# Kernel tuning notes

Measured on AMD Instinct MI355X. Metric: run time of the kernel, lower is better.

## Reference

```python
import jax, jax.numpy as jnp
import numpy as np

IN_FEATURES = 1024
OUT_FEATURES = 1024
BATCH = 32
SEQ = 1024
EPS = 1e-8


def setup_inputs() -> dict:
    key = jax.random.key(0)
    k1, k2, k3 = jax.random.split(key, 3)
    Efou = jax.random.normal(k1, (BATCH, SEQ, IN_FEATURES), dtype=jnp.float32)
    y = jax.random.normal(k2, (BATCH, IN_FEATURES), dtype=jnp.float32)
    weight = jax.random.normal(k3, (IN_FEATURES, OUT_FEATURES), dtype=jnp.float32)
    return {"Efou": Efou, "y": y, "weight": weight}


def reference(Efou, y, weight):
    # scale = 1/sqrt(in_features)
    scale = 1.0 / np.sqrt(np.float32(weight.shape[0]))
    ys = y * scale  # (b, i) == per-sample column scaling of weight
    # Demodulation norm: sum_i (scale*W[i,o]*y[b,i])^2 = (ys^2) @ (W^2)
    d = jax.lax.rsqrt(jnp.einsum('bi,io->bo', ys * ys, weight * weight) + EPS)  # (b, o)
    # Efou @ (scale*W*y*d) == ((Efou*ys) @ W) * d  -- same math, avoids (b,i,o) weight
    out = jnp.einsum('bsi,io->bso', Efou * ys[:, None, :], weight) * d[:, None, :]
    return out
```

## Files before the change

### kernel.cpp

```cpp
#include <hip/hip_runtime.h>

#define AS1 __attribute__((address_space(1)))
#define AS3 __attribute__((address_space(3)))

typedef __bf16 bf16x8 __attribute__((ext_vector_type(8)));
typedef float f32x4 __attribute__((ext_vector_type(4)));
typedef unsigned short ushort8 __attribute__((ext_vector_type(8)));

__device__ __forceinline__ unsigned short f2bf(float f) {
  union { float f; unsigned u; } v; v.f = f;
  unsigned u = v.u;
  unsigned r = (u + 0x7fffu + ((u >> 16) & 1u)) >> 16;
  return (unsigned short)r;
}

__global__ __launch_bounds__(256) void prep_kernel(const float* __restrict__ y,
                                                   const float* __restrict__ W,
                                                   float* __restrict__ partial,
                                                   unsigned short* __restrict__ WT) {
  __shared__ float ysq[32][32];
  const int o = blockIdx.x * 256 + threadIdx.x;
  const int i0 = blockIdx.y * 32;
  for (int e = threadIdx.x; e < 1024; e += 256) {
    int il = e >> 5, b = e & 31;
    float t = y[b * 1024 + i0 + il] * 0.03125f;
    ysq[il][b] = t * t;
  }
  __syncthreads();

  f32x4 acc[8] = {};
  ushort8 wb[4];
#pragma unroll
  for (int il = 0; il < 32; ++il) {
    float w = W[(size_t)(i0 + il) * 1024 + o];
    wb[il >> 3][il & 7] = f2bf(w);
    float w2 = w * w;
#pragma unroll
    for (int b4 = 0; b4 < 8; ++b4) {
      f32x4 q = *(const f32x4*)&ysq[il][b4 * 4];
#pragma unroll
      for (int k = 0; k < 4; ++k) acc[b4][k] = fmaf(q[k], w2, acc[b4][k]);
    }
  }
  unsigned short* wt = WT + (size_t)o * 1024 + i0;
#pragma unroll
  for (int q = 0; q < 4; ++q) *(ushort8*)(wt + q * 8) = wb[q];
  float* p = partial + (size_t)blockIdx.y * 32768 + o;
#pragma unroll
  for (int b4 = 0; b4 < 8; ++b4)
#pragma unroll
    for (int k = 0; k < 4; ++k) p[(b4 * 4 + k) * 1024] = acc[b4][k];
}

__global__ __launch_bounds__(256) void dcalc_b_kernel(const float* __restrict__ partial,
                                                      float* __restrict__ dmod) {
  const int bo = blockIdx.x * 256 + threadIdx.x;
  float acc = 0.f;
#pragma unroll 8
  for (int is = 0; is < 32; ++is) acc += partial[(size_t)is * 32768 + bo];
  dmod[bo] = rsqrtf(acc + 1e-8f);
}

#define NT 16
#define LDS_TILE 65536

#define BAR __builtin_amdgcn_s_barrier()
#define LGKM0 asm volatile("s_waitcnt lgkmcnt(0)" ::: "memory")
#define VM(n) asm volatile("s_waitcnt vmcnt(" #n ")" ::: "memory")
#define SCHB __builtin_amdgcn_sched_barrier(0)
#define PRIO(x) __builtin_amdgcn_s_setprio(x)

#define STG_B(r, t, dst)                                                     \
  __builtin_amdgcn_global_load_lds(                                          \
      (const AS1 void*)(Ws + (size_t)(r) * 64 * 2048 + (t) * 128),           \
      (AS3 void*)((dst) + 32768 + (r) * 8192 + sldso), 16, 0, 0)

#define A_ISSUE(t)                                                           \
  {                                                                          \
    const float* asrc = Efou + (size_t)(m0 + argp * 4) * 1024 + (t) * 64 + k8; \
    _Pragma("unroll") for (int rr = 0; rr < 4; ++rr) {                       \
      pa[rr][0] = *(const f32x4*)(asrc + rr * 1024);                         \
      pa[rr][1] = *(const f32x4*)(asrc + rr * 1024 + 4);                     \
    }                                                                        \
    yv[0] = *(const f32x4*)(ysS + (t) * 64 + k8);                            \
    yv[1] = *(const f32x4*)(ysS + (t) * 64 + k8 + 4);                        \
  }

#define ACVT_ROW(dst, rr)                                                    \
  {                                                                          \
    const int row = argp * 4 + (rr);                                         \
    bf16x8 ov;                                                               \
    _Pragma("unroll") for (int q = 0; q < 4; ++q) {                          \
      ov[q] = (__bf16)(pa[rr][0][q] * yv[0][q]);                             \
      ov[q + 4] = (__bf16)(pa[rr][1][q] * yv[1][q]);                         \
    }                                                                        \
    *(bf16x8*)((dst) + row * 128 + ((kslot * 16) ^ ((row & 7) << 4))) = ov;  \
  }

#define RD_A(mh, mi, kk)                                                     \
  (*(const bf16x8*)(Ab + (wr * 128 + ((mh) * 4 + (mi)) * 16 + l15) * 128 +   \
                    ((((kk) * 64 + lhi * 16)) ^ swz_rd)))
#define RD_B(nh, ni, kk)                                                     \
  (*(const bf16x8*)(Bb + (wc * 64 + ((nh) * 2 + (ni)) * 16 + l15) * 128 +    \
                    ((((kk) * 64 + lhi * 16)) ^ swz_rd)))

#define LD_A(mh)                                                             \
  { _Pragma("unroll") for (int mi = 0; mi < 4; ++mi)                         \
      _Pragma("unroll") for (int kk = 0; kk < 2; ++kk)                       \
        a[mi][kk] = RD_A(mh, mi, kk); }
#define LD_B(nh)                                                             \
  { _Pragma("unroll") for (int ni = 0; ni < 2; ++ni)                         \
      _Pragma("unroll") for (int kk = 0; kk < 2; ++kk)                       \
        bfr[ni][kk] = RD_B(nh, ni, kk); }

#define MM(mh, nh)                                                           \
  do {                                                                       \
    _Pragma("unroll") for (int mi = 0; mi < 4; ++mi)                         \
      _Pragma("unroll") for (int ni = 0; ni < 2; ++ni)                       \
        _Pragma("unroll") for (int kk = 0; kk < 2; ++kk)                     \
          acc[(mh) * 4 + mi][(nh) * 2 + ni] =                                \
              __builtin_amdgcn_mfma_f32_16x16x32_bf16(                       \
                  a[mi][kk], bfr[ni][kk], acc[(mh) * 4 + mi][(nh) * 2 + ni], \
                  0, 0, 0);                                                  \
  } while (0)

__global__ __launch_bounds__(512, 2) void gemmf5_kernel(
    const float* __restrict__ Efou, const float* __restrict__ y,
    const unsigned short* __restrict__ WT, const float* __restrict__ dmod,
    float* __restrict__ out) {
  extern __shared__ char lds[];
  float* ysS = (float*)(lds + 2 * LDS_TILE);

  const int tid = threadIdx.x;
  const int bid = blockIdx.x;
  const int wg = (bid & 7) * 64 + (bid >> 3);
  const int bm = wg >> 2, bn = wg & 3;
  const int m0 = bm * 256, n0 = bn * 256;
  const int b = m0 >> 10;

  const int w = tid >> 6, l = tid & 63;
  const int wr = w >> 2, wc = w & 3;
  const int l15 = l & 15, lhi = l >> 4;
  const int swz_rd = (l15 & 7) << 4;

  const int kslot = tid & 7;
  const int k8 = kslot * 8;
  const int argp = tid >> 3;

  const int srow = tid >> 3;
  const int scb = ((tid & 7) << 4) ^ ((srow & 7) << 4);
  const char* Ws = (const char*)WT + (size_t)(n0 + srow) * 2048 + scb;
  const int sldso = tid * 16;

  f32x4 acc[8][4] = {};
  bf16x8 a[4][2], bfr[2][2];
  f32x4 pa[4][2], yv[2];

  {
    float2 yy = *(const float2*)(y + b * 1024 + tid * 2);
    ysS[2 * tid] = yy.x * 0.03125f;
    ysS[2 * tid + 1] = yy.y * 0.03125f;
  }
  __syncthreads();
  {
    char* d0 = lds;
    STG_B(0, 0, d0); STG_B(1, 0, d0); STG_B(2, 0, d0); STG_B(3, 0, d0);
    A_ISSUE(0);
    ACVT_ROW(d0, 0); ACVT_ROW(d0, 1); ACVT_ROW(d0, 2); ACVT_ROW(d0, 3);
  }
  VM(0); LGKM0; BAR;

  for (int t = 0; t < NT - 1; ++t) {
    const char* Ab = lds + (t & 1) * LDS_TILE;
    const char* Bb = Ab + 32768;
    char* dN = lds + ((t & 1) ^ 1) * LDS_TILE;
    const int t1 = t + 1;
    LD_A(0); LD_B(0);
    A_ISSUE(t1);
    STG_B(0, t1, dN); STG_B(1, t1, dN);
    BAR; LGKM0; SCHB; PRIO(1); MM(0, 0); PRIO(0); SCHB; BAR;
    LD_B(1);
    STG_B(2, t1, dN); STG_B(3, t1, dN);
    BAR; LGKM0; SCHB; PRIO(1); MM(0, 1); PRIO(0); SCHB; BAR;
    LD_A(1); LD_B(0);
    BAR; LGKM0; SCHB; PRIO(1);
    ACVT_ROW(dN, 0); ACVT_ROW(dN, 1);
    MM(1, 0);
    PRIO(0); SCHB; BAR;
    LD_B(1);
    BAR; LGKM0; SCHB; PRIO(1);
    ACVT_ROW(dN, 2); ACVT_ROW(dN, 3);
    MM(1, 1);
    PRIO(0); SCHB;
    VM(0);
    LGKM0;
    BAR;
  }

  {
    const char* Ab = lds + ((NT - 1) & 1) * LDS_TILE;
    const char* Bb = Ab + 32768;
    LD_A(0); LD_B(0);
    BAR; LGKM0; SCHB; PRIO(1); MM(0, 0); PRIO(0); SCHB; BAR;
    LD_B(1);
    BAR; LGKM0; SCHB; PRIO(1); MM(0, 1); PRIO(0); SCHB; BAR;
    LD_A(1); LD_B(0);
    BAR; LGKM0; SCHB; PRIO(1); MM(1, 0); PRIO(0); SCHB; BAR;
    LD_B(1);
    BAR; LGKM0; SCHB; PRIO(1); MM(1, 1); PRIO(0); SCHB;
  }

  const int col0 = n0 + wc * 64 + l15;
  float dv[4];
#pragma unroll
  for (int nf = 0; nf < 4; ++nf) dv[nf] = dmod[b * 1024 + col0 + nf * 16];
#pragma unroll
  for (int mf = 0; mf < 8; ++mf) {
#pragma unroll
    for (int j = 0; j < 4; ++j) {
      const int row = m0 + wr * 128 + mf * 16 + lhi * 4 + j;
      float* orow = out + (size_t)row * 1024 + col0;
#pragma unroll
      for (int nf = 0; nf < 4; ++nf) orow[nf * 16] = acc[mf][nf][j] * dv[nf];
    }
  }
}

extern "C" void kernel_launch(void* const* d_in, const int* in_sizes, int n_in,
                              void* d_out, int out_size, void* d_ws, size_t ws_size,
                              hipStream_t stream) {
  const float* Efou = (const float*)d_in[0];
  const float* y    = (const float*)d_in[1];
  const float* W    = (const float*)d_in[2];
  float* out = (float*)d_out;

  unsigned short* WT = (unsigned short*)d_ws;
  float* dpart       = (float*)(WT + (size_t)1024 * 1024);
  float* dmod        = dpart + (size_t)32 * 32768;

  hipFuncSetAttribute((const void*)gemmf5_kernel,
                      hipFuncAttributeMaxDynamicSharedMemorySize, 135168);

  prep_kernel<<<dim3(4, 32), 256, 0, stream>>>(y, W, dpart, WT);
  dcalc_b_kernel<<<128, 256, 0, stream>>>(dpart, dmod);
  gemmf5_kernel<<<512, 512, 135168, stream>>>(Efou, y, WT, dmod, out);
}
```

Measured before the change: 127.9 us.

## Load all B fragments once per tile and remove intermediate barriers

Loads both halves of the B fragments into registers at the start of each K-tile instead of reloading them for each A half. This halves the B LDS reads, and most intermediate barriers and waits in the main loop are removed, so MFMA phases run back-to-back. The cost is more vector registers held live, which could cause spills under the 2-blocks-per-CU launch bound, and less fine-grained interleaving of global staging with compute.

```diff
diff --git a/kernel.cpp b/kernel.cpp
--- a/kernel.cpp
+++ b/kernel.cpp
@@ -108,10 +108,11 @@
   { _Pragma("unroll") for (int mi = 0; mi < 4; ++mi)                         \
       _Pragma("unroll") for (int kk = 0; kk < 2; ++kk)                       \
         a[mi][kk] = RD_A(mh, mi, kk); }
-#define LD_B(nh)                                                             \
-  { _Pragma("unroll") for (int ni = 0; ni < 2; ++ni)                         \
-      _Pragma("unroll") for (int kk = 0; kk < 2; ++kk)                       \
-        bfr[ni][kk] = RD_B(nh, ni, kk); }
+#define LD_B_ALL                                                             \
+  { _Pragma("unroll") for (int nh = 0; nh < 2; ++nh)                         \
+      _Pragma("unroll") for (int ni = 0; ni < 2; ++ni)                       \
+        _Pragma("unroll") for (int kk = 0; kk < 2; ++kk)                     \
+          bfr[nh][ni][kk] = RD_B(nh, ni, kk); }
 
 #define MM(mh, nh)                                                           \
   do {                                                                       \
@@ -120,11 +121,11 @@
         _Pragma("unroll") for (int kk = 0; kk < 2; ++kk)                     \
           acc[(mh) * 4 + mi][(nh) * 2 + ni] =                                \
               __builtin_amdgcn_mfma_f32_16x16x32_bf16(                       \
-                  a[mi][kk], bfr[ni][kk], acc[(mh) * 4 + mi][(nh) * 2 + ni], \
-                  0, 0, 0);                                                  \
+                  a[mi][kk], bfr[nh][ni][kk],                                \
+                  acc[(mh) * 4 + mi][(nh) * 2 + ni], 0, 0, 0);               \
   } while (0)
 
-__global__ __launch_bounds__(512, 2) void gemmf5_kernel(
+__global__ __launch_bounds__(512, 2) void gemmf6_kernel(
     const float* __restrict__ Efou, const float* __restrict__ y,
     const unsigned short* __restrict__ WT, const float* __restrict__ dmod,
     float* __restrict__ out) {
@@ -153,7 +154,7 @@
   const int sldso = tid * 16;
 
   f32x4 acc[8][4] = {};
-  bf16x8 a[4][2], bfr[2][2];
+  bf16x8 a[4][2], bfr[2][2][2];
   f32x4 pa[4][2], yv[2];
 
   {
@@ -175,20 +176,14 @@
     const char* Bb = Ab + 32768;
     char* dN = lds + ((t & 1) ^ 1) * LDS_TILE;
     const int t1 = t + 1;
-    LD_A(0); LD_B(0);
+    LD_A(0); LD_B_ALL;
     A_ISSUE(t1);
-    STG_B(0, t1, dN); STG_B(1, t1, dN);
-    BAR; LGKM0; SCHB; PRIO(1); MM(0, 0); PRIO(0); SCHB; BAR;
-    LD_B(1);
-    STG_B(2, t1, dN); STG_B(3, t1, dN);
-    BAR; LGKM0; SCHB; PRIO(1); MM(0, 1); PRIO(0); SCHB; BAR;
-    LD_A(1); LD_B(0);
-    BAR; LGKM0; SCHB; PRIO(1);
+    STG_B(0, t1, dN); STG_B(1, t1, dN); STG_B(2, t1, dN); STG_B(3, t1, dN);
+    BAR; LGKM0; SCHB; PRIO(1); MM(0, 0); MM(0, 1); PRIO(0); SCHB; BAR;
+    LD_A(1);
+    SCHB; PRIO(1);
     ACVT_ROW(dN, 0); ACVT_ROW(dN, 1);
     MM(1, 0);
-    PRIO(0); SCHB; BAR;
-    LD_B(1);
-    BAR; LGKM0; SCHB; PRIO(1);
     ACVT_ROW(dN, 2); ACVT_ROW(dN, 3);
     MM(1, 1);
     PRIO(0); SCHB;
@@ -200,14 +195,10 @@
   {
     const char* Ab = lds + ((NT - 1) & 1) * LDS_TILE;
     const char* Bb = Ab + 32768;
-    LD_A(0); LD_B(0);
-    BAR; LGKM0; SCHB; PRIO(1); MM(0, 0); PRIO(0); SCHB; BAR;
-    LD_B(1);
-    BAR; LGKM0; SCHB; PRIO(1); MM(0, 1); PRIO(0); SCHB; BAR;
-    LD_A(1); LD_B(0);
-    BAR; LGKM0; SCHB; PRIO(1); MM(1, 0); PRIO(0); SCHB; BAR;
-    LD_B(1);
-    BAR; LGKM0; SCHB; PRIO(1); MM(1, 1); PRIO(0); SCHB;
+    LD_A(0); LD_B_ALL;
+    BAR; LGKM0; SCHB; PRIO(1); MM(0, 0); MM(0, 1); PRIO(0); SCHB;
+    LD_A(1);
+    LGKM0; SCHB; PRIO(1); MM(1, 0); MM(1, 1); PRIO(0); SCHB;
   }
 
   const int col0 = n0 + wc * 64 + l15;
@@ -238,10 +229,10 @@
   float* dpart       = (float*)(WT + (size_t)1024 * 1024);
   float* dmod        = dpart + (size_t)32 * 32768;
 
-  hipFuncSetAttribute((const void*)gemmf5_kernel,
+  hipFuncSetAttribute((const void*)gemmf6_kernel,
                       hipFuncAttributeMaxDynamicSharedMemorySize, 135168);
 
   prep_kernel<<<dim3(4, 32), 256, 0, stream>>>(y, W, dpart, WT);
   dcalc_b_kernel<<<128, 256, 0, stream>>>(dpart, dmod);
-  gemmf5_kernel<<<512, 512, 135168, stream>>>(Efou, y, WT, dmod, out);
-}
+  gemmf6_kernel<<<512, 512, 135168, stream>>>(Efou, y, WT, dmod, out);
+}
```

Result: no change. 130.2 us (+1.8%).
